# Kernel tuning notes

Hardware: AMD Instinct MI355X
Metric: run time of the kernel (lower is better)

Reference implementation:

```python
import jax, jax.numpy as jnp
import numpy as np

N, E, De, Dv = 40000, 8000, 32, 8   # nodes, hyperedges, edge degree, node degree
D, Q, EIG, VOC, NC = 256, 256, 64, 1000, 40  # vertex/edge dim, query dim, eig dim, centrality vocab, classes
LN_EPS = 1e-5


def _linear(x, W, b):
    return x @ W + b


def _layernorm(x, g, b):
    mu = jnp.mean(x, axis=-1, keepdims=True)
    var = jnp.mean(jnp.square(x - mu), axis=-1, keepdims=True)
    return (x - mu) * jax.lax.rsqrt(var + LN_EPS) * g + b


def setup_inputs() -> dict:
    key = jax.random.key(0)
    ks = iter(jax.random.split(key, 64))
    def nrm(shape, s=0.02):
        return (jax.random.normal(next(ks), shape, jnp.float32) * s).astype(jnp.float32)
    inp = {
        'vfeat': jax.random.normal(next(ks), (N, D), jnp.float32),
        'efeat': jax.random.normal(next(ks), (E, D), jnp.float32),
        'eign_vec': jax.random.normal(next(ks), (N, EIG), jnp.float32),
        'feat_v_gcn': jax.random.normal(next(ks), (N, D), jnp.float32),
        'cent1': jax.random.uniform(next(ks), (E, De), jnp.float32),
        'cent2': jax.random.uniform(next(ks), (N, Dv), jnp.float32),
        'cent_idx': jax.random.randint(next(ks), (N,), 0, VOC),
        'uniq_idx': jax.random.randint(next(ks), (N,), 0, VOC),
        'edge2node': jax.random.randint(next(ks), (E, De), 0, N),
        'node2edge': jax.random.randint(next(ks), (N, Dv), 0, E),
        # learned parameters (W: [in, out])
        'W_vtx': nrm((D, D)), 'b_vtx': jnp.zeros((D,), jnp.float32),
        'W_pe': nrm((EIG, D)), 'b_pe': jnp.zeros((D,), jnp.float32),
        'cs_emb': nrm((VOC, D)), 'un_emb': nrm((VOC, D)),
        'W_kv': nrm((D, Q)), 'b_kv': jnp.zeros((Q,), jnp.float32),
        'W_vv': nrm((D, D)), 'b_vv': jnp.zeros((D,), jnp.float32),
        'W_qe': nrm((D, Q)), 'b_qe': jnp.zeros((Q,), jnp.float32),
        'W_ke': nrm((D, Q)), 'b_ke': jnp.zeros((Q,), jnp.float32),
        'W_ve': nrm((D, D)), 'b_ve': jnp.zeros((D,), jnp.float32),
        'W_qv': nrm((D, Q)), 'b_qv': jnp.zeros((Q,), jnp.float32),
        'W_l1': nrm((D, Q)), 'b_l1': jnp.zeros((Q,), jnp.float32),
        'W_l2': nrm((Q, D)), 'b_l2': jnp.zeros((D,), jnp.float32),
        'W_l3': nrm((D, Q)), 'b_l3': jnp.zeros((Q,), jnp.float32),
        'W_l4': nrm((Q, D)), 'b_l4': jnp.zeros((D,), jnp.float32),
        'ln1_g': jnp.ones((D,), jnp.float32), 'ln1_b': jnp.zeros((D,), jnp.float32),
        'ln2_g': jnp.ones((D,), jnp.float32), 'ln2_b': jnp.zeros((D,), jnp.float32),
        'W_cls': nrm((D, NC)), 'b_cls': jnp.zeros((NC,), jnp.float32),
    }
    return inp


def _forward(vfeat, efeat, eign_vec, feat_v_gcn, cent1, cent2,
             W_vtx, b_vtx, W_pe, b_pe, cs_emb, un_emb,
             W_kv, b_kv, W_vv, b_vv, W_qe, b_qe, W_ke, b_ke, W_ve, b_ve, W_qv, b_qv,
             W_l1, b_l1, W_l2, b_l2, W_l3, b_l3, W_l4, b_l4,
             ln1_g, ln1_b, ln2_g, ln2_b, W_cls, b_cls,
             cent_idx, uniq_idx, edge2node, node2edge):
    scale = 1.0 / np.sqrt(float(W_kv.shape[1]))  # 1/sqrt(query_dim)
    # first_layer feature assembly: vtx_lin_1layer + PE + GCN + centrality/uniqueness embeddings
    feat_v = (_linear(vfeat, W_vtx, b_vtx) + _linear(eign_vec, W_pe, b_pe)
              + feat_v_gcn + cs_emb[cent_idx] + un_emb[uniq_idx])
    feat_e = efeat

    # ---- stage 1: hyperedges attend over member nodes ('in' etype) ----
    k_n = _linear(feat_v, W_kv, b_kv)              # [N,Q]
    v_n = _linear(feat_v, W_vv, b_vv)              # [N,D]
    q_e = _linear(feat_e, W_qe, b_qe)              # [E,Q]
    km = k_n[edge2node]                            # [E,De,Q]
    attn = jax.nn.leaky_relu(jnp.einsum('edq,eq->ed', km, q_e), 0.01) * scale
    score = jax.nn.softmax(attn + cent1, axis=1)   # centrality-biased softmax (k-core + clustering)
    h_e = jnp.einsum('ed,edc->ec', score, v_n[edge2node])  # [E,D]
    x_e = _layernorm(h_e + feat_e, ln1_g, ln1_b)
    f_e = _linear(jax.nn.relu(_linear(x_e, W_l1, b_l1)), W_l2, b_l2)
    feat_e = _layernorm(f_e + x_e, ln1_g, ln1_b)

    # ---- stage 2: nodes attend over incident hyperedges ('con' etype) ----
    k_e = _linear(feat_e, W_ke, b_ke)              # [E,Q]
    v_e = _linear(feat_e, W_ve, b_ve)              # [E,D]
    q_v = _linear(feat_v, W_qv, b_qv)              # [N,Q]
    km2 = k_e[node2edge]                           # [N,Dv,Q]
    attn2 = jax.nn.leaky_relu(jnp.einsum('ndq,nq->nd', km2, q_v), 0.01) * scale
    score2 = jax.nn.softmax(attn2 + cent2, axis=1)
    h_v = jnp.einsum('nd,ndc->nc', score2, v_e[node2edge])  # [N,D]
    x_v = _layernorm(h_v + feat_v, ln2_g, ln2_b)
    f_v = _linear(jax.nn.relu(_linear(x_v, W_l3, b_l3)), W_l4, b_l4)
    feat_v = _layernorm(f_v + x_v, ln2_g, ln2_b)

    # last_layer classification head (dropout is identity in eval)
    return _linear(feat_v, W_cls, b_cls)           # [N,NC]


def reference(vfeat, efeat, eign_vec, feat_v_gcn, cent1, cent2,
              cent_idx, uniq_idx, edge2node, node2edge,
              W_vtx, b_vtx, W_pe, b_pe, cs_emb, un_emb,
              W_kv, b_kv, W_vv, b_vv, W_qe, b_qe, W_ke, b_ke, W_ve, b_ve, W_qv, b_qv,
              W_l1, b_l1, W_l2, b_l2, W_l3, b_l3, W_l4, b_l4,
              ln1_g, ln1_b, ln2_g, ln2_b, W_cls, b_cls):
    return _forward(vfeat, efeat, eign_vec, feat_v_gcn, cent1, cent2,
                    W_vtx, b_vtx, W_pe, b_pe, cs_emb, un_emb,
                    W_kv, b_kv, W_vv, b_vv, W_qe, b_qe, W_ke, b_ke, W_ve, b_ve, W_qv, b_qv,
                    W_l1, b_l1, W_l2, b_l2, W_l3, b_l3, W_l4, b_l4,
                    ln1_g, ln1_b, ln2_g, ln2_b, W_cls, b_cls,
                    cent_idx, uniq_idx, edge2node, node2edge)
```

## Files before the change

kernel.cpp:

```cpp
#include <hip/hip_runtime.h>
#include <hip/hip_bf16.h>
#include <cstddef>

#define N_NODES 40000
#define N_EDGES 8000
#define DE 32
#define DV 8
#define DIM 256
#define QDIM 256
#define EIGD 64
#define NCLS 40
#define LN_EPS 1e-5f
#define ATT_SCALE 0.0625f

typedef unsigned short u16;
typedef unsigned int u32;
using i16x8 = __attribute__((ext_vector_type(8))) short;
using f32x4 = __attribute__((ext_vector_type(4))) float;

__device__ inline u16 f2b(float f) {
    union { float f; u32 u; } c; c.f = f;
    u32 u = c.u + 0x7FFF + ((c.u >> 16) & 1);
    return (u16)(u >> 16);
}
__device__ inline float b2f(u16 b) {
    union { u32 u; float f; } c; c.u = (u32)b << 16;
    return c.f;
}

__device__ inline void gload_lds16(const u16* g, u16* l) {
    __builtin_amdgcn_global_load_lds(
        (const __attribute__((address_space(1))) void*)g,
        (__attribute__((address_space(3))) void*)l, 16, 0, 0);
}

#define VMCNT12 asm volatile("s_waitcnt vmcnt(12)" ::: "memory")
#define VMCNT10 asm volatile("s_waitcnt vmcnt(10)" ::: "memory")
#define VMCNT6  asm volatile("s_waitcnt vmcnt(6)" ::: "memory")
#define VMCNT5  asm volatile("s_waitcnt vmcnt(5)" ::: "memory")
#define VMCNT0  asm volatile("s_waitcnt vmcnt(0)" ::: "memory")
#define LGKM0   asm volatile("s_waitcnt lgkmcnt(0)" ::: "memory")

__global__ __launch_bounds__(256) void prep_weights(
    const float* w0, const float* w1, const float* w2, const float* w3,
    const float* w4, const float* w5, const float* w6, const float* w7,
    const float* w8, const float* w9, const float* w10, const float* w11,
    const float* w12, u16* __restrict__ pool)
{
    const float* srcs[13] = {w0,w1,w2,w3,w4,w5,w6,w7,w8,w9,w10,w11,w12};
    const int Ks[13]  = {256,64,256,256,256,256,256,256,256,256,256,256,256};
    const int Nds[13] = {256,256,256,256,256,256,256,256,256,256,256,256,40};
    const int id = blockIdx.z;
    const float* W = srcs[id];
    u16* Wt = pool + (size_t)id * 65536;
    const int K = Ks[id], Nd = Nds[id];
    const int k0 = blockIdx.x * 32, n0 = blockIdx.y * 32;
    if (k0 >= K || n0 >= Nd) return;

    __shared__ float tile[32][33];
    const int x = threadIdx.x & 31, y4 = (threadIdx.x >> 5) * 4;
#pragma unroll
    for (int j = 0; j < 4; j++) {
        int k = k0 + y4 + j;
        tile[y4 + j][x] = (k < K && (n0 + x) < Nd) ? W[(size_t)k * Nd + n0 + x] : 0.f;
    }
    __syncthreads();
#pragma unroll
    for (int j = 0; j < 4; j++) {
        int n = n0 + y4 + j;
        if (n < Nd && (k0 + x) < K)
            Wt[(size_t)n * K + k0 + x] = f2b(tile[x][y4 + j]);
    }
}

template <int EPI, int AMODE, int NT>
__global__ __launch_bounds__(256, 2) void gemmN(
    const void* __restrict__ Av, const u16* __restrict__ Wt,
    const float* __restrict__ bias0, const float* __restrict__ bias1,
    const float* __restrict__ bias2,
    void* __restrict__ Cv, int Nd)
{
    __shared__ u16 Asm[3][64 * 64];
    __shared__ u16 Bsm[3][128 * 64];
    const int t = threadIdx.x;
    const int lane = t & 63, w = t >> 6;
    const int wr = w >> 1, wc = w & 1;
    const int row0 = blockIdx.y * 64, col0 = blockIdx.x * 128;

    f32x4 acc[2][4] = {};

    const int srow = lane >> 3;
    const int sblk = ((lane & 7) ^ srow) * 8;
    const int fr = lane & 15, h = lane >> 4;
    const int lsw = fr & 7;

    float4 farA[2][2][2];

    auto stage_load = [&](int kt) {
        const int buf = kt % 3;
        const int k0 = kt << 6;
        if constexpr (AMODE == 0) {
#pragma unroll
            for (int i = 0; i < 2; i++) {
                const int r = w * 16 + i * 8;
                gload_lds16((const u16*)Av + (size_t)(row0 + r + srow) * 256 + k0 + sblk,
                            &Asm[buf][r * 64]);
            }
        } else {
#pragma unroll
            for (int i = 0; i < 2; i++) {
                const int r = w * 16 + i * 8;
                const float* ap = (const float*)Av + (size_t)(row0 + r + srow) * 256 + k0 + sblk;
                farA[kt & 1][i][0] = *(const float4*)ap;
                farA[kt & 1][i][1] = *(const float4*)(ap + 4);
            }
        }
#pragma unroll
        for (int i = 0; i < 4; i++) {
            const int r = w * 32 + i * 8;
            int ng = col0 + r + srow; if (ng > Nd - 1) ng = Nd - 1;
            gload_lds16(Wt + (size_t)ng * 256 + k0 + sblk, &Bsm[buf][r * 64]);
        }
    };
    auto stage_write = [&](int kt) {
        const int buf = kt % 3;
#pragma unroll
        for (int i = 0; i < 2; i++) {
            const int r = w * 16 + i * 8;
            float4 f0 = farA[kt & 1][i][0], f1 = farA[kt & 1][i][1];
            i16x8 v;
            v[0] = (short)f2b(f0.x); v[1] = (short)f2b(f0.y);
            v[2] = (short)f2b(f0.z); v[3] = (short)f2b(f0.w);
            v[4] = (short)f2b(f1.x); v[5] = (short)f2b(f1.y);
            v[6] = (short)f2b(f1.z); v[7] = (short)f2b(f1.w);
            *(i16x8*)&Asm[buf][(r + srow) * 64 + (lane & 7) * 8] = v;
        }
    };

    stage_load(0);
    if (NT > 1) stage_load(1);
    if constexpr (AMODE != 0) stage_write(0);

#pragma unroll
    for (int kt = 0; kt < NT; ++kt) {
        const int buf = kt % 3;
        if (kt + 2 < NT) stage_load(kt + 2);
        if constexpr (AMODE != 0) {
            if (kt + 1 < NT) stage_write(kt + 1);
            else { VMCNT0; }
        } else {
            if (kt + 2 < NT) { VMCNT12; }
            else if (kt + 1 < NT) { VMCNT6; }
            else { VMCNT0; }
        }
        __builtin_amdgcn_s_barrier();

        i16x8 af[2][2], bfr[2][4];
#pragma unroll
        for (int kk = 0; kk < 2; kk++) {
#pragma unroll
            for (int m = 0; m < 2; m++)
                af[kk][m] = *(const i16x8*)&Asm[buf][(wr * 32 + m * 16 + fr) * 64 +
                                                    ((kk * 4 + h) ^ lsw) * 8];
#pragma unroll
            for (int n = 0; n < 4; n++)
                bfr[kk][n] = *(const i16x8*)&Bsm[buf][(wc * 64 + n * 16 + fr) * 64 +
                                                     ((kk * 4 + h) ^ lsw) * 8];
        }
        LGKM0;
        __builtin_amdgcn_sched_barrier(0);
        __builtin_amdgcn_s_barrier();

#pragma unroll
        for (int kk = 0; kk < 2; kk++)
#pragma unroll
            for (int m = 0; m < 2; m++)
#pragma unroll
                for (int n = 0; n < 4; n++)
                    acc[m][n] = __builtin_amdgcn_mfma_f32_16x16x32_bf16(
                        af[kk][m], bfr[kk][n], acc[m][n], 0, 0, 0);
    }

    const int seg = (int)(blockIdx.x >> 1);
    const float* bp = (seg == 0) ? bias0 : ((seg == 1) ? bias1 : bias2);
#pragma unroll
    for (int m = 0; m < 2; m++) {
#pragma unroll
        for (int j = 0; j < 4; j++) {
            const int grow = row0 + wr * 32 + m * 16 + h * 4 + j;
#pragma unroll
            for (int n = 0; n < 4; n++) {
                const int gcol = col0 + wc * 64 + n * 16 + fr;
                if (EPI == 4 && gcol >= Nd) continue;
                float v = acc[m][n][j] + bp[gcol & 255];
                if constexpr (EPI == 1) v = fmaxf(v, 0.f);
                if constexpr (EPI == 4)
                    ((float*)Cv)[(size_t)grow * Nd + gcol] = v;
                else
                    ((u16*)Cv)[(size_t)grow * Nd + gcol] = f2b(v);
            }
        }
    }
}

template <int EPI, int AMODE, int NT>
__global__ __launch_bounds__(256, 2) void gemmW(
    const void* __restrict__ Av, const float* __restrict__ A2,
    const u16* __restrict__ Wt, const u16* __restrict__ Wt2,
    const float* __restrict__ bias0, const float* __restrict__ bias1,
    const u16* __restrict__ resid,
    const float* __restrict__ gcn, const float* __restrict__ emb1,
    const float* __restrict__ emb2, const int* __restrict__ idx1,
    const int* __restrict__ idx2, const float* __restrict__ lng,
    const float* __restrict__ lnb, u16* __restrict__ Cv)
{
    __shared__ u16 Asm[3][64 * 32];
    __shared__ u16 Bsm[3][256 * 32];
    const int t = threadIdx.x;
    const int lane = t & 63, w = t >> 6;
    const int row0 = blockIdx.y * 64;

    f32x4 acc[4][4] = {};

    const int srow = lane >> 2;
    const int sblk = ((lane & 3) ^ ((lane >> 3) & 3)) * 8;
    const int fr = lane & 15, h = lane >> 4;
    const int rsw = (fr >> 1) & 3;

    float4 farA[2][2];

    auto stage_load = [&](int kt) {
        const int buf = kt % 3;
        const int k0 = kt << 5;
        const bool tail = (AMODE == 2) && (k0 >= 256);
        if constexpr (AMODE == 0) {
            gload_lds16((const u16*)Av + (size_t)(row0 + w * 16 + srow) * 256 + k0 + sblk,
                        &Asm[buf][(w * 16) * 32]);
        } else {
            const float* ap = tail
                ? A2 + (size_t)(row0 + w * 16 + srow) * 64 + (k0 - 256) + sblk
                : (const float*)Av + (size_t)(row0 + w * 16 + srow) * 256 + k0 + sblk;
            farA[kt & 1][0] = *(const float4*)ap;
            farA[kt & 1][1] = *(const float4*)(ap + 4);
        }
#pragma unroll
        for (int i = 0; i < 4; i++) {
            const int r = w * 64 + i * 16;
            const u16* gp = tail ? Wt2 + (size_t)(r + srow) * 64 + (k0 - 256) + sblk
                                 : Wt + (size_t)(r + srow) * 256 + k0 + sblk;
            gload_lds16(gp, &Bsm[buf][r * 32]);
        }
    };
    auto stage_write = [&](int kt) {
        const int buf = kt % 3;
        float4 f0 = farA[kt & 1][0], f1 = farA[kt & 1][1];
        i16x8 v;
        v[0] = (short)f2b(f0.x); v[1] = (short)f2b(f0.y);
        v[2] = (short)f2b(f0.z); v[3] = (short)f2b(f0.w);
        v[4] = (short)f2b(f1.x); v[5] = (short)f2b(f1.y);
        v[6] = (short)f2b(f1.z); v[7] = (short)f2b(f1.w);
        *(i16x8*)&Asm[buf][(w * 16 + srow) * 32 + (lane & 3) * 8] = v;
    };

    stage_load(0);
    if (NT > 1) stage_load(1);
    if constexpr (AMODE != 0) stage_write(0);

#pragma unroll
    for (int kt = 0; kt < NT; ++kt) {
        const int buf = kt % 3;
        if (kt + 2 < NT) stage_load(kt + 2);
        if constexpr (AMODE != 0) {
            if (kt + 1 < NT) stage_write(kt + 1);
            else { VMCNT0; }
        } else {
            if (kt + 2 < NT) { VMCNT10; }
            else if (kt + 1 < NT) { VMCNT5; }
            else { VMCNT0; }
        }
        __builtin_amdgcn_s_barrier();

        i16x8 af[4], bfr[4];
#pragma unroll
        for (int m = 0; m < 4; m++)
            af[m] = *(const i16x8*)&Asm[buf][(m * 16 + fr) * 32 + (h ^ rsw) * 8];
#pragma unroll
        for (int n = 0; n < 4; n++)
            bfr[n] = *(const i16x8*)&Bsm[buf][(w * 64 + n * 16 + fr) * 32 + (h ^ rsw) * 8];
        LGKM0;
        __builtin_amdgcn_sched_barrier(0);
        __builtin_amdgcn_s_barrier();

#pragma unroll
        for (int m = 0; m < 4; m++)
#pragma unroll
            for (int n = 0; n < 4; n++)
                acc[m][n] = __builtin_amdgcn_mfma_f32_16x16x32_bf16(
                    af[m], bfr[n], acc[m][n], 0, 0, 0);
    }

    if constexpr (EPI == 5) {
        float* redS = (float*)&Asm[0][0];
        float* redQ = redS + 256;
#pragma unroll
        for (int m = 0; m < 4; m++) {
#pragma unroll
            for (int j = 0; j < 4; j++) {
                const int grow = row0 + m * 16 + h * 4 + j;
                float s = 0.f, q = 0.f;
#pragma unroll
                for (int n = 0; n < 4; n++) {
                    const int gcol = w * 64 + n * 16 + fr;
                    float v = acc[m][n][j] + bias0[gcol] +
                              b2f(resid[(size_t)grow * 256 + gcol]);
                    acc[m][n][j] = v;
                    s += v; q += v * v;
                }
#pragma unroll
                for (int off = 1; off < 16; off <<= 1) {
                    s += __shfl_xor(s, off, 64);
                    q += __shfl_xor(q, off, 64);
                }
                if (fr == 0) {
                    redS[(m * 16 + h * 4 + j) * 4 + w] = s;
                    redQ[(m * 16 + h * 4 + j) * 4 + w] = q;
                }
            }
        }
        __syncthreads();
#pragma unroll
        for (int m = 0; m < 4; m++) {
#pragma unroll
            for (int j = 0; j < 4; j++) {
                const int r = m * 16 + h * 4 + j;
                const int grow = row0 + r;
                float4 s4 = *(const float4*)&redS[r * 4];
                float4 q4 = *(const float4*)&redQ[r * 4];
                float mu = (s4.x + s4.y + s4.z + s4.w) * (1.f / DIM);
                float var = (q4.x + q4.y + q4.z + q4.w) * (1.f / DIM) - mu * mu;
                float rr = rsqrtf(var + LN_EPS);
#pragma unroll
                for (int n = 0; n < 4; n++) {
                    const int gcol = w * 64 + n * 16 + fr;
                    float y = (acc[m][n][j] - mu) * rr * lng[gcol] + lnb[gcol];
                    Cv[(size_t)grow * 256 + gcol] = f2b(y);
                }
            }
        }
    } else {
#pragma unroll
        for (int m = 0; m < 4; m++) {
#pragma unroll
            for (int j = 0; j < 4; j++) {
                const int grow = row0 + m * 16 + h * 4 + j;
                const int i1 = idx1[grow], i2 = idx2[grow];
#pragma unroll
                for (int n = 0; n < 4; n++) {
                    const int gcol = w * 64 + n * 16 + fr;
                    float v = acc[m][n][j] + bias0[gcol] + bias1[gcol];
                    v += gcn[(size_t)grow * 256 + gcol];
                    v += emb1[(size_t)i1 * 256 + gcol];
                    v += emb2[(size_t)i2 * 256 + gcol];
                    Cv[(size_t)grow * 256 + gcol] = f2b(v);
                }
            }
        }
    }
}

__global__ __launch_bounds__(256) void edge_attn(
    const u16* __restrict__ KVQn, const u16* __restrict__ QE,
    const float* __restrict__ efeat,
    const int* __restrict__ e2n, const float* __restrict__ cent1,
    const float* __restrict__ g, const float* __restrict__ bb,
    u16* __restrict__ XE)
{
    const int lane = threadIdx.x & 63, w = threadIdx.x >> 6;
    const int e = blockIdx.x * 4 + w;
    const int c4 = lane * 4;

    ushort4 q4 = *(const ushort4*)&QE[(size_t)e * QDIM + c4];
    const float q0 = b2f(q4.x), q1 = b2f(q4.y), q2 = b2f(q4.z), q3 = b2f(q4.w);

    int4 rv[8];
#pragma unroll
    for (int i = 0; i < 8; i++)
        rv[i] = *(const int4*)&e2n[(size_t)e * DE + i * 4];
    int rows[DE];
#pragma unroll
    for (int i = 0; i < 8; i++) {
        rows[i * 4 + 0] = rv[i].x; rows[i * 4 + 1] = rv[i].y;
        rows[i * 4 + 2] = rv[i].z; rows[i * 4 + 3] = rv[i].w;
    }

    float p[DE];
#pragma unroll
    for (int g0 = 0; g0 < DE; g0 += 16) {
        ushort4 k4[16];
#pragma unroll
        for (int j = 0; j < 16; j++)
            k4[j] = *(const ushort4*)&KVQn[(size_t)rows[g0 + j] * 768 + c4];
#pragma unroll
        for (int j = 0; j < 16; j++)
            p[g0 + j] = q0 * b2f(k4[j].x) + q1 * b2f(k4[j].y)
                      + q2 * b2f(k4[j].z) + q3 * b2f(k4[j].w);
    }
#pragma unroll
    for (int off = 32; off; off >>= 1)
#pragma unroll
        for (int d = 0; d < DE; d++)
            p[d] += __shfl_xor(p[d], off, 64);

    float4 cv[8];
#pragma unroll
    for (int i = 0; i < 8; i++)
        cv[i] = *(const float4*)&cent1[(size_t)e * DE + i * 4];
    float cent[DE];
#pragma unroll
    for (int i = 0; i < 8; i++) {
        cent[i * 4 + 0] = cv[i].x; cent[i * 4 + 1] = cv[i].y;
        cent[i * 4 + 2] = cv[i].z; cent[i * 4 + 3] = cv[i].w;
    }
#pragma unroll
    for (int d = 0; d < DE; d++)
        p[d] = (p[d] > 0.f ? p[d] : 0.01f * p[d]) * ATT_SCALE + cent[d];

    float mx = p[0];
#pragma unroll
    for (int d = 1; d < DE; d++) mx = fmaxf(mx, p[d]);
    float s = 0.f;
#pragma unroll
    for (int d = 0; d < DE; d++) { p[d] = __expf(p[d] - mx); s += p[d]; }
    const float inv = 1.f / s;
#pragma unroll
    for (int d = 0; d < DE; d++) p[d] *= inv;

    float a0 = 0.f, a1 = 0.f, a2 = 0.f, a3 = 0.f;
#pragma unroll
    for (int g0 = 0; g0 < DE; g0 += 16) {
        ushort4 v4[16];
#pragma unroll
        for (int j = 0; j < 16; j++)
            v4[j] = *(const ushort4*)&KVQn[(size_t)rows[g0 + j] * 768 + 256 + c4];
#pragma unroll
        for (int j = 0; j < 16; j++) {
            const float sd = p[g0 + j];
            a0 = fmaf(sd, b2f(v4[j].x), a0); a1 = fmaf(sd, b2f(v4[j].y), a1);
            a2 = fmaf(sd, b2f(v4[j].z), a2); a3 = fmaf(sd, b2f(v4[j].w), a3);
        }
    }
    float4 ef = *(const float4*)&efeat[(size_t)e * DIM + c4];
    float x0 = a0 + ef.x, x1 = a1 + ef.y, x2 = a2 + ef.z, x3 = a3 + ef.w;

    float mu = x0 + x1 + x2 + x3;
#pragma unroll
    for (int off = 32; off; off >>= 1) mu += __shfl_xor(mu, off, 64);
    mu *= (1.f / DIM);
    float d0 = x0 - mu, d1 = x1 - mu, d2 = x2 - mu, d3 = x3 - mu;
    float var = d0 * d0 + d1 * d1 + d2 * d2 + d3 * d3;
#pragma unroll
    for (int off = 32; off; off >>= 1) var += __shfl_xor(var, off, 64);
    var *= (1.f / DIM);
    float r = rsqrtf(var + LN_EPS);
    float4 gv = *(const float4*)&g[c4];
    float4 bv = *(const float4*)&bb[c4];
    ushort4 o;
    o.x = f2b(d0 * r * gv.x + bv.x); o.y = f2b(d1 * r * gv.y + bv.y);
    o.z = f2b(d2 * r * gv.z + bv.z); o.w = f2b(d3 * r * gv.w + bv.w);
    *(ushort4*)&XE[(size_t)e * DIM + c4] = o;
}

__global__ __launch_bounds__(256) void node_attn(
    const u16* __restrict__ KVe, const u16* __restrict__ KVQn,
    const u16* __restrict__ FV,
    const int* __restrict__ n2e, const float* __restrict__ cent2,
    const float* __restrict__ g, const float* __restrict__ bb,
    u16* __restrict__ XV)
{
    const int lane = threadIdx.x & 63, w = threadIdx.x >> 6;
    const int na = blockIdx.x * 8 + w * 2, nb = na + 1;
    const int c4 = lane * 4;

    ushort4 qa4 = *(const ushort4*)&KVQn[(size_t)na * 768 + 512 + c4];
    ushort4 qb4 = *(const ushort4*)&KVQn[(size_t)nb * 768 + 512 + c4];
    const float qa0 = b2f(qa4.x), qa1 = b2f(qa4.y), qa2 = b2f(qa4.z), qa3 = b2f(qa4.w);
    const float qb0 = b2f(qb4.x), qb1 = b2f(qb4.y), qb2 = b2f(qb4.z), qb3 = b2f(qb4.w);

    int4 r0 = *(const int4*)&n2e[(size_t)na * DV];
    int4 r1 = *(const int4*)&n2e[(size_t)na * DV + 4];
    int4 r2 = *(const int4*)&n2e[(size_t)nb * DV];
    int4 r3 = *(const int4*)&n2e[(size_t)nb * DV + 4];
    int rA[8] = {r0.x, r0.y, r0.z, r0.w, r1.x, r1.y, r1.z, r1.w};
    int rB[8] = {r2.x, r2.y, r2.z, r2.w, r3.x, r3.y, r3.z, r3.w};

    ushort4 kA[8], vA[8], kB[8], vB[8];
#pragma unroll
    for (int d = 0; d < DV; d++) {
        const u16* b = KVe + (size_t)rA[d] * 512 + c4;
        kA[d] = *(const ushort4*)b; vA[d] = *(const ushort4*)(b + 256);
    }
#pragma unroll
    for (int d = 0; d < DV; d++) {
        const u16* b = KVe + (size_t)rB[d] * 512 + c4;
        kB[d] = *(const ushort4*)b; vB[d] = *(const ushort4*)(b + 256);
    }

    float pA[8], pB[8];
#pragma unroll
    for (int d = 0; d < DV; d++) {
        pA[d] = qa0 * b2f(kA[d].x) + qa1 * b2f(kA[d].y)
              + qa2 * b2f(kA[d].z) + qa3 * b2f(kA[d].w);
        pB[d] = qb0 * b2f(kB[d].x) + qb1 * b2f(kB[d].y)
              + qb2 * b2f(kB[d].z) + qb3 * b2f(kB[d].w);
    }
#pragma unroll
    for (int off = 32; off; off >>= 1) {
#pragma unroll
        for (int d = 0; d < DV; d++) {
            pA[d] += __shfl_xor(pA[d], off, 64);
            pB[d] += __shfl_xor(pB[d], off, 64);
        }
    }
    float4 cA0 = *(const float4*)&cent2[(size_t)na * DV];
    float4 cA1 = *(const float4*)&cent2[(size_t)na * DV + 4];
    float4 cB0 = *(const float4*)&cent2[(size_t)nb * DV];
    float4 cB1 = *(const float4*)&cent2[(size_t)nb * DV + 4];
    float cA[8] = {cA0.x, cA0.y, cA0.z, cA0.w, cA1.x, cA1.y, cA1.z, cA1.w};
    float cB[8] = {cB0.x, cB0.y, cB0.z, cB0.w, cB1.x, cB1.y, cB1.z, cB1.w};
#pragma unroll
    for (int d = 0; d < DV; d++) {
        pA[d] = (pA[d] > 0.f ? pA[d] : 0.01f * pA[d]) * ATT_SCALE + cA[d];
        pB[d] = (pB[d] > 0.f ? pB[d] : 0.01f * pB[d]) * ATT_SCALE + cB[d];
    }
    float mA = pA[0], mB = pB[0];
#pragma unroll
    for (int d = 1; d < DV; d++) { mA = fmaxf(mA, pA[d]); mB = fmaxf(mB, pB[d]); }
    float sA = 0.f, sB = 0.f;
#pragma unroll
    for (int d = 0; d < DV; d++) {
        pA[d] = __expf(pA[d] - mA); sA += pA[d];
        pB[d] = __expf(pB[d] - mB); sB += pB[d];
    }
    const float iA = 1.f / sA, iB = 1.f / sB;

    float a0 = 0.f, a1 = 0.f, a2 = 0.f, a3 = 0.f;
    float b0 = 0.f, b1 = 0.f, b2 = 0.f, b3 = 0.f;
#pragma unroll
    for (int d = 0; d < DV; d++) {
        const float sa = pA[d] * iA, sb = pB[d] * iB;
        a0 = fmaf(sa, b2f(vA[d].x), a0); a1 = fmaf(sa, b2f(vA[d].y), a1);
        a2 = fmaf(sa, b2f(vA[d].z), a2); a3 = fmaf(sa, b2f(vA[d].w), a3);
        b0 = fmaf(sb, b2f(vB[d].x), b0); b1 = fmaf(sb, b2f(vB[d].y), b1);
        b2 = fmaf(sb, b2f(vB[d].z), b2); b3 = fmaf(sb, b2f(vB[d].w), b3);
    }
    ushort4 fa = *(const ushort4*)&FV[(size_t)na * DIM + c4];
    ushort4 fb = *(const ushort4*)&FV[(size_t)nb * DIM + c4];
    float xa0 = a0 + b2f(fa.x), xa1 = a1 + b2f(fa.y);
    float xa2 = a2 + b2f(fa.z), xa3 = a3 + b2f(fa.w);
    float xb0 = b0 + b2f(fb.x), xb1 = b1 + b2f(fb.y);
    float xb2 = b2 + b2f(fb.z), xb3 = b3 + b2f(fb.w);

    float muA = xa0 + xa1 + xa2 + xa3, muB = xb0 + xb1 + xb2 + xb3;
#pragma unroll
    for (int off = 32; off; off >>= 1) {
        muA += __shfl_xor(muA, off, 64);
        muB += __shfl_xor(muB, off, 64);
    }
    muA *= (1.f / DIM); muB *= (1.f / DIM);
    float da0 = xa0 - muA, da1 = xa1 - muA, da2 = xa2 - muA, da3 = xa3 - muA;
    float db0 = xb0 - muB, db1 = xb1 - muB, db2 = xb2 - muB, db3 = xb3 - muB;
    float vA_ = da0 * da0 + da1 * da1 + da2 * da2 + da3 * da3;
    float vB_ = db0 * db0 + db1 * db1 + db2 * db2 + db3 * db3;
#pragma unroll
    for (int off = 32; off; off >>= 1) {
        vA_ += __shfl_xor(vA_, off, 64);
        vB_ += __shfl_xor(vB_, off, 64);
    }
    const float rA_ = rsqrtf(vA_ * (1.f / DIM) + LN_EPS);
    const float rB_ = rsqrtf(vB_ * (1.f / DIM) + LN_EPS);
    float4 gv = *(const float4*)&g[c4];
    float4 bv = *(const float4*)&bb[c4];
    ushort4 oa, ob;
    oa.x = f2b(da0 * rA_ * gv.x + bv.x); oa.y = f2b(da1 * rA_ * gv.y + bv.y);
    oa.z = f2b(da2 * rA_ * gv.z + bv.z); oa.w = f2b(da3 * rA_ * gv.w + bv.w);
    ob.x = f2b(db0 * rB_ * gv.x + bv.x); ob.y = f2b(db1 * rB_ * gv.y + bv.y);
    ob.z = f2b(db2 * rB_ * gv.z + bv.z); ob.w = f2b(db3 * rB_ * gv.w + bv.w);
    *(ushort4*)&XV[(size_t)na * DIM + c4] = oa;
    *(ushort4*)&XV[(size_t)nb * DIM + c4] = ob;
}

extern "C" void kernel_launch(void* const* d_in, const int* in_sizes, int n_in,
                              void* d_out, int out_size, void* d_ws, size_t ws_size,
                              hipStream_t stream)
{
    const float* vfeat  = (const float*)d_in[0];
    const float* efeat  = (const float*)d_in[1];
    const float* eign   = (const float*)d_in[2];
    const float* gcn    = (const float*)d_in[3];
    const float* cent1  = (const float*)d_in[4];
    const float* cent2  = (const float*)d_in[5];
    const int*   cidx   = (const int*)d_in[6];
    const int*   uidx   = (const int*)d_in[7];
    const int*   e2n    = (const int*)d_in[8];
    const int*   n2e    = (const int*)d_in[9];
    const float* W_vtx  = (const float*)d_in[10]; const float* b_vtx = (const float*)d_in[11];
    const float* W_pe   = (const float*)d_in[12]; const float* b_pe  = (const float*)d_in[13];
    const float* cs_emb = (const float*)d_in[14]; const float* un_emb= (const float*)d_in[15];
    const float* W_kv   = (const float*)d_in[16]; const float* b_kv  = (const float*)d_in[17];
    const float* W_vv   = (const float*)d_in[18]; const float* b_vv  = (const float*)d_in[19];
    const float* W_qe   = (const float*)d_in[20]; const float* b_qe  = (const float*)d_in[21];
    const float* W_ke   = (const float*)d_in[22]; const float* b_ke  = (const float*)d_in[23];
    const float* W_ve   = (const float*)d_in[24]; const float* b_ve  = (const float*)d_in[25];
    const float* W_qv   = (const float*)d_in[26]; const float* b_qv  = (const float*)d_in[27];
    const float* W_l1   = (const float*)d_in[28]; const float* b_l1  = (const float*)d_in[29];
    const float* W_l2   = (const float*)d_in[30]; const float* b_l2  = (const float*)d_in[31];
    const float* W_l3   = (const float*)d_in[32]; const float* b_l3  = (const float*)d_in[33];
    const float* W_l4   = (const float*)d_in[34]; const float* b_l4  = (const float*)d_in[35];
    const float* ln1_g  = (const float*)d_in[36]; const float* ln1_b = (const float*)d_in[37];
    const float* ln2_g  = (const float*)d_in[38]; const float* ln2_b = (const float*)d_in[39];
    const float* W_cls  = (const float*)d_in[40]; const float* b_cls = (const float*)d_in[41];
    float* out = (float*)d_out;

    const size_t NE = (size_t)N_NODES * DIM;
    const size_t EE = (size_t)N_EDGES * DIM;
    u16* ws = (u16*)d_ws;
    u16* FVb  = ws;
    u16* KVQn = FVb + NE;
    u16* B2   = KVQn + 3 * NE;
    u16* T0   = B2 + NE;
    u16* QEb  = T0 + NE;
    u16* XE   = QEb + EE;
    u16* TE   = XE + EE;
    u16* FE   = TE + EE;
    u16* KVe  = FE + EE;
    u16* Wp   = KVe + 2 * EE;
    u16* Wt_vtx = Wp +  0 * 65536;
    u16* Wt_pe  = Wp +  1 * 65536;
    u16* Wt_kvq = Wp +  2 * 65536;
    u16* Wt_qe  = Wp +  5 * 65536;
    u16* Wt_kve = Wp +  6 * 65536;
    u16* Wt_l1  = Wp +  8 * 65536;
    u16* Wt_l2  = Wp +  9 * 65536;
    u16* Wt_l3  = Wp + 10 * 65536;
    u16* Wt_l4  = Wp + 11 * 65536;
    u16* Wt_cls = Wp + 12 * 65536;

    const dim3 blk(256);
    const dim3 gW(8, 8, 13);
    const dim3 gAsm(1, N_NODES / 64);
    const dim3 gKVQ(6, N_NODES / 64);
    const dim3 gQE(2, N_EDGES / 64);
    const dim3 gL1(2, N_EDGES / 64);
    const dim3 gLNE(1, N_EDGES / 64);
    const dim3 gKVe(4, N_EDGES / 64);
    const dim3 gL3(2, N_NODES / 64);
    const dim3 gLNN(1, N_NODES / 64);
    const dim3 gCl(1, N_NODES / 64);

    prep_weights<<<gW, blk, 0, stream>>>(
        W_vtx, W_pe, W_kv, W_vv, W_qv, W_qe, W_ke, W_ve,
        W_l1, W_l2, W_l3, W_l4, W_cls, Wp);

    gemmW<3, 2, 10><<<gAsm, blk, 0, stream>>>(vfeat, eign, Wt_vtx, Wt_pe,
        b_vtx, b_pe, nullptr, gcn, cs_emb, un_emb, cidx, uidx,
        nullptr, nullptr, FVb);

    gemmN<0, 0, 4><<<gKVQ, blk, 0, stream>>>(FVb, Wt_kvq,
        b_kv, b_vv, b_qv, KVQn, 768);
    gemmN<0, 1, 4><<<gQE, blk, 0, stream>>>(efeat, Wt_qe,
        b_qe, b_qe, b_qe, QEb, 256);
    edge_attn<<<N_EDGES / 4, blk, 0, stream>>>(KVQn, QEb, efeat, e2n, cent1,
        ln1_g, ln1_b, XE);
    gemmN<1, 0, 4><<<gL1, blk, 0, stream>>>(XE, Wt_l1,
        b_l1, b_l1, b_l1, TE, 256);
    gemmW<5, 0, 8><<<gLNE, blk, 0, stream>>>(TE, nullptr, Wt_l2, nullptr,
        b_l2, nullptr, XE, nullptr, nullptr, nullptr, nullptr, nullptr,
        ln1_g, ln1_b, FE);

    gemmN<0, 0, 4><<<gKVe, blk, 0, stream>>>(FE, Wt_kve,
        b_ke, b_ve, b_ve, KVe, 512);
    node_attn<<<N_NODES / 8, blk, 0, stream>>>(KVe, KVQn, FVb, n2e, cent2,
        ln2_g, ln2_b, B2);
    gemmN<1, 0, 4><<<gL3, blk, 0, stream>>>(B2, Wt_l3,
        b_l3, b_l3, b_l3, T0, 256);
    gemmW<5, 0, 8><<<gLNN, blk, 0, stream>>>(T0, nullptr, Wt_l4, nullptr,
        b_l4, nullptr, B2, nullptr, nullptr, nullptr, nullptr, nullptr,
        ln2_g, ln2_b, FVb);

    gemmN<4, 0, 4><<<gCl, blk, 0, stream>>>(FVb, Wt_cls,
        b_cls, b_cls, b_cls, out, NCLS);
}
```

Measured before the change: 260.6 us.

## Fuse FFN, residual LayerNorm and following projection into one kernel

Adds an ffn_fused kernel that, for a 64-row tile, computes linear+ReLU, the second linear, residual add and LayerNorm, then the next projection (edge K/V or node classifier). The intermediate activations stay in shared memory instead of making round trips through global buffers, replacing three launches per side with one. The trade-off is a large shared-memory footprint and fewer blocks: a single block per 64 rows, only 125 blocks on the edge side. That could lower parallelism compared with the previous multi-column grids.

```diff
diff --git a/kernel.cpp b/kernel.cpp
--- a/kernel.cpp
+++ b/kernel.cpp
@@ -38,6 +38,7 @@
 #define VMCNT10 asm volatile("s_waitcnt vmcnt(10)" ::: "memory")
 #define VMCNT6  asm volatile("s_waitcnt vmcnt(6)" ::: "memory")
 #define VMCNT5  asm volatile("s_waitcnt vmcnt(5)" ::: "memory")
+#define VMCNT4  asm volatile("s_waitcnt vmcnt(4)" ::: "memory")
 #define VMCNT0  asm volatile("s_waitcnt vmcnt(0)" ::: "memory")
 #define LGKM0   asm volatile("s_waitcnt lgkmcnt(0)" ::: "memory")
 
@@ -363,6 +364,252 @@
                     v += emb2[(size_t)i2 * 256 + gcol];
                     Cv[(size_t)grow * 256 + gcol] = f2b(v);
                 }
+            }
+        }
+    }
+}
+
+#define MST 264
+template <int TAIL>
+__global__ __launch_bounds__(256, 2) void ffn_fused(
+    const u16* __restrict__ X, const u16* __restrict__ Wt1,
+    const float* __restrict__ b1, const u16* __restrict__ Wt2,
+    const float* __restrict__ b2, const float* __restrict__ lng,
+    const float* __restrict__ lnb, const u16* __restrict__ WtT,
+    const float* __restrict__ bT0, const float* __restrict__ bT1,
+    void* __restrict__ outp)
+{
+    __shared__ __align__(16) u16 Asm[2][64 * 32];
+    __shared__ __align__(16) u16 Bsm[2][256 * 32];
+    __shared__ __align__(16) u16 Msm[64 * MST];
+    const int t = threadIdx.x;
+    const int lane = t & 63, w = t >> 6;
+    const int row0 = blockIdx.x * 64;
+
+    const int srow = lane >> 2;
+    const int sblk = ((lane & 3) ^ ((lane >> 3) & 3)) * 8;
+    const int fr = lane & 15, h = lane >> 4;
+    const int rsw = (fr >> 1) & 3;
+
+    f32x4 acc[4][4] = {};
+
+    auto stageA = [&](int buf, int kt) {
+        gload_lds16(X + (size_t)(row0 + w * 16 + srow) * 256 + (kt << 5) + sblk,
+                    &Asm[buf][(w * 16) * 32]);
+    };
+    auto stageB = [&](int buf, int kt, const u16* W) {
+#pragma unroll
+        for (int i = 0; i < 4; i++) {
+            const int r = w * 64 + i * 16;
+            gload_lds16(W + (size_t)(r + srow) * 256 + (kt << 5) + sblk,
+                        &Bsm[buf][r * 32]);
+        }
+    };
+
+    stageA(0, 0); stageB(0, 0, Wt1);
+#pragma unroll
+    for (int kt = 0; kt < 8; ++kt) {
+        const int buf = kt & 1;
+        if (kt < 7) { stageA(buf ^ 1, kt + 1); stageB(buf ^ 1, kt + 1, Wt1); VMCNT5; }
+        else { VMCNT0; }
+        __builtin_amdgcn_s_barrier();
+
+        i16x8 af[4], bfr[4];
+#pragma unroll
+        for (int m = 0; m < 4; m++)
+            af[m] = *(const i16x8*)&Asm[buf][(m * 16 + fr) * 32 + (h ^ rsw) * 8];
+#pragma unroll
+        for (int n = 0; n < 4; n++)
+            bfr[n] = *(const i16x8*)&Bsm[buf][(w * 64 + n * 16 + fr) * 32 + (h ^ rsw) * 8];
+        LGKM0;
+        __builtin_amdgcn_sched_barrier(0);
+        __builtin_amdgcn_s_barrier();
+
+#pragma unroll
+        for (int m = 0; m < 4; m++)
+#pragma unroll
+            for (int n = 0; n < 4; n++)
+                acc[m][n] = __builtin_amdgcn_mfma_f32_16x16x32_bf16(
+                    af[m], bfr[n], acc[m][n], 0, 0, 0);
+    }
+    {
+        float b1v[4];
+#pragma unroll
+        for (int n = 0; n < 4; n++) b1v[n] = b1[w * 64 + n * 16 + fr];
+#pragma unroll
+        for (int m = 0; m < 4; m++)
+#pragma unroll
+            for (int j = 0; j < 4; j++) {
+                const int row = m * 16 + h * 4 + j;
+#pragma unroll
+                for (int n = 0; n < 4; n++) {
+                    const int col = w * 64 + n * 16 + fr;
+                    float v = fmaxf(acc[m][n][j] + b1v[n], 0.f);
+                    Msm[row * MST + col] = f2b(v);
+                    acc[m][n][j] = 0.f;
+                }
+            }
+    }
+    __syncthreads();
+
+    stageB(0, 0, Wt2);
+#pragma unroll
+    for (int kt = 0; kt < 8; ++kt) {
+        const int buf = kt & 1;
+        if (kt < 7) { stageB(buf ^ 1, kt + 1, Wt2); VMCNT4; }
+        else { VMCNT0; }
+        __builtin_amdgcn_s_barrier();
+
+        i16x8 af[4], bfr[4];
+#pragma unroll
+        for (int m = 0; m < 4; m++)
+            af[m] = *(const i16x8*)&Msm[(m * 16 + fr) * MST + (kt << 5) + h * 8];
+#pragma unroll
+        for (int n = 0; n < 4; n++)
+            bfr[n] = *(const i16x8*)&Bsm[buf][(w * 64 + n * 16 + fr) * 32 + (h ^ rsw) * 8];
+        LGKM0;
+        __builtin_amdgcn_sched_barrier(0);
+        __builtin_amdgcn_s_barrier();
+
+#pragma unroll
+        for (int m = 0; m < 4; m++)
+#pragma unroll
+            for (int n = 0; n < 4; n++)
+                acc[m][n] = __builtin_amdgcn_mfma_f32_16x16x32_bf16(
+                    af[m], bfr[n], acc[m][n], 0, 0, 0);
+    }
+    {
+        float* redS = (float*)&Asm[0][0];
+        float* redQ = redS + 256;
+#pragma unroll
+        for (int m = 0; m < 4; m++) {
+#pragma unroll
+            for (int j = 0; j < 4; j++) {
+                const int grow = row0 + m * 16 + h * 4 + j;
+                float s = 0.f, q = 0.f;
+#pragma unroll
+                for (int n = 0; n < 4; n++) {
+                    const int gcol = w * 64 + n * 16 + fr;
+                    float v = acc[m][n][j] + b2[gcol] +
+                              b2f(X[(size_t)grow * 256 + gcol]);
+                    acc[m][n][j] = v;
+                    s += v; q += v * v;
+                }
+#pragma unroll
+                for (int off = 1; off < 16; off <<= 1) {
+                    s += __shfl_xor(s, off, 64);
+                    q += __shfl_xor(q, off, 64);
+                }
+                if (fr == 0) {
+                    redS[(m * 16 + h * 4 + j) * 4 + w] = s;
+                    redQ[(m * 16 + h * 4 + j) * 4 + w] = q;
+                }
+            }
+        }
+        __syncthreads();
+#pragma unroll
+        for (int m = 0; m < 4; m++) {
+#pragma unroll
+            for (int j = 0; j < 4; j++) {
+                const int r = m * 16 + h * 4 + j;
+                float4 s4 = *(const float4*)&redS[r * 4];
+                float4 q4 = *(const float4*)&redQ[r * 4];
+                float mu = (s4.x + s4.y + s4.z + s4.w) * (1.f / DIM);
+                float var = (q4.x + q4.y + q4.z + q4.w) * (1.f / DIM) - mu * mu;
+                float rr = rsqrtf(var + LN_EPS);
+#pragma unroll
+                for (int n = 0; n < 4; n++) {
+                    const int gcol = w * 64 + n * 16 + fr;
+                    float y = (acc[m][n][j] - mu) * rr * lng[gcol] + lnb[gcol];
+                    acc[m][n][j] = y;
+                }
+            }
+        }
+        __syncthreads();
+#pragma unroll
+        for (int m = 0; m < 4; m++)
+#pragma unroll
+            for (int j = 0; j < 4; j++) {
+                const int row = m * 16 + h * 4 + j;
+#pragma unroll
+                for (int n = 0; n < 4; n++)
+                    Msm[row * MST + (w * 64 + n * 16 + fr)] = f2b(acc[m][n][j]);
+            }
+    }
+    VMCNT0;
+    __syncthreads();
+
+    if constexpr (TAIL == 0) {
+        u16* KVe = (u16*)outp;
+#pragma unroll
+        for (int half = 0; half < 2; half++) {
+            const u16* Wb = WtT + (size_t)half * 256 * 256;
+            const float* bT = half ? bT1 : bT0;
+#pragma unroll
+            for (int m = 0; m < 4; m++)
+#pragma unroll
+                for (int n = 0; n < 4; n++)
+                    acc[m][n] = f32x4{0.f, 0.f, 0.f, 0.f};
+            stageB(0, 0, Wb);
+#pragma unroll
+            for (int kt = 0; kt < 8; ++kt) {
+                const int buf = kt & 1;
+                if (kt < 7) { stageB(buf ^ 1, kt + 1, Wb); VMCNT4; }
+                else { VMCNT0; }
+                __builtin_amdgcn_s_barrier();
+
+                i16x8 af[4], bfr[4];
+#pragma unroll
+                for (int m = 0; m < 4; m++)
+                    af[m] = *(const i16x8*)&Msm[(m * 16 + fr) * MST + (kt << 5) + h * 8];
+#pragma unroll
+                for (int n = 0; n < 4; n++)
+                    bfr[n] = *(const i16x8*)&Bsm[buf][(w * 64 + n * 16 + fr) * 32 + (h ^ rsw) * 8];
+                LGKM0;
+                __builtin_amdgcn_sched_barrier(0);
+                __builtin_amdgcn_s_barrier();
+
+#pragma unroll
+                for (int m = 0; m < 4; m++)
+#pragma unroll
+                    for (int n = 0; n < 4; n++)
+                        acc[m][n] = __builtin_amdgcn_mfma_f32_16x16x32_bf16(
+                            af[m], bfr[n], acc[m][n], 0, 0, 0);
+            }
+#pragma unroll
+            for (int m = 0; m < 4; m++)
+#pragma unroll
+                for (int j = 0; j < 4; j++) {
+                    const int grow = row0 + m * 16 + h * 4 + j;
+#pragma unroll
+                    for (int n = 0; n < 4; n++) {
+                        const int gcol = w * 64 + n * 16 + fr;
+                        KVe[(size_t)grow * 512 + half * 256 + gcol] =
+                            f2b(acc[m][n][j] + bT[gcol]);
+                    }
+                }
+        }
+    } else {
+        float* out = (float*)outp;
+        f32x4 acc3[3] = {};
+#pragma unroll
+        for (int kk = 0; kk < 8; kk++) {
+            i16x8 af = *(const i16x8*)&Msm[(w * 16 + fr) * MST + kk * 32 + h * 8];
+#pragma unroll
+            for (int n = 0; n < 3; n++) {
+                int br = n * 16 + fr; if (br > NCLS - 1) br = NCLS - 1;
+                i16x8 bfr = *(const i16x8*)(WtT + (size_t)br * 256 + kk * 32 + h * 8);
+                acc3[n] = __builtin_amdgcn_mfma_f32_16x16x32_bf16(af, bfr, acc3[n], 0, 0, 0);
+            }
+        }
+#pragma unroll
+        for (int n = 0; n < 3; n++) {
+            const int gcol = n * 16 + fr;
+            if (gcol >= NCLS) continue;
+#pragma unroll
+            for (int j = 0; j < 4; j++) {
+                const int grow = row0 + w * 16 + h * 4 + j;
+                out[(size_t)grow * NCLS + gcol] = acc3[n][j] + bT0[gcol];
             }
         }
     }
@@ -627,12 +874,9 @@
     u16* FVb  = ws;
     u16* KVQn = FVb + NE;
     u16* B2   = KVQn + 3 * NE;
-    u16* T0   = B2 + NE;
-    u16* QEb  = T0 + NE;
+    u16* QEb  = B2 + NE;
     u16* XE   = QEb + EE;
-    u16* TE   = XE + EE;
-    u16* FE   = TE + EE;
-    u16* KVe  = FE + EE;
+    u16* KVe  = XE + EE;
     u16* Wp   = KVe + 2 * EE;
     u16* Wt_vtx = Wp +  0 * 65536;
     u16* Wt_pe  = Wp +  1 * 65536;
@@ -650,12 +894,6 @@
     const dim3 gAsm(1, N_NODES / 64);
     const dim3 gKVQ(6, N_NODES / 64);
     const dim3 gQE(2, N_EDGES / 64);
-    const dim3 gL1(2, N_EDGES / 64);
-    const dim3 gLNE(1, N_EDGES / 64);
-    const dim3 gKVe(4, N_EDGES / 64);
-    const dim3 gL3(2, N_NODES / 64);
-    const dim3 gLNN(1, N_NODES / 64);
-    const dim3 gCl(1, N_NODES / 64);
 
     prep_weights<<<gW, blk, 0, stream>>>(
         W_vtx, W_pe, W_kv, W_vv, W_qv, W_qe, W_ke, W_ve,
@@ -671,22 +909,11 @@
         b_qe, b_qe, b_qe, QEb, 256);
     edge_attn<<<N_EDGES / 4, blk, 0, stream>>>(KVQn, QEb, efeat, e2n, cent1,
         ln1_g, ln1_b, XE);
-    gemmN<1, 0, 4><<<gL1, blk, 0, stream>>>(XE, Wt_l1,
-        b_l1, b_l1, b_l1, TE, 256);
-    gemmW<5, 0, 8><<<gLNE, blk, 0, stream>>>(TE, nullptr, Wt_l2, nullptr,
-        b_l2, nullptr, XE, nullptr, nullptr, nullptr, nullptr, nullptr,
-        ln1_g, ln1_b, FE);
-
-    gemmN<0, 0, 4><<<gKVe, blk, 0, stream>>>(FE, Wt_kve,
-        b_ke, b_ve, b_ve, KVe, 512);
+    ffn_fused<0><<<N_EDGES / 64, blk, 0, stream>>>(XE, Wt_l1, b_l1,
+        Wt_l2, b_l2, ln1_g, ln1_b, Wt_kve, b_ke, b_ve, KVe);
+
     node_attn<<<N_NODES / 8, blk, 0, stream>>>(KVe, KVQn, FVb, n2e, cent2,
         ln2_g, ln2_b, B2);
-    gemmN<1, 0, 4><<<gL3, blk, 0, stream>>>(B2, Wt_l3,
-        b_l3, b_l3, b_l3, T0, 256);
-    gemmW<5, 0, 8><<<gLNN, blk, 0, stream>>>(T0, nullptr, Wt_l4, nullptr,
-        b_l4, nullptr, B2, nullptr, nullptr, nullptr, nullptr, nullptr,
-        ln2_g, ln2_b, FVb);
-
-    gemmN<4, 0, 4><<<gCl, blk, 0, stream>>>(FVb, Wt_cls,
-        b_cls, b_cls, b_cls, out, NCLS);
+    ffn_fused<1><<<N_NODES / 64, blk, 0, stream>>>(B2, Wt_l3, b_l3,
+        Wt_l4, b_l4, ln2_g, ln2_b, Wt_cls, b_cls, nullptr, out);
 }
```

New measurement: 239.3 us. 1.09x faster.
